# Kernel optimization log

Measured on AMD Instinct MI355X. Metric: run time of the kernel, lower is better.

## Reference

```python
import jax, jax.numpy as jnp
import numpy as np

B = 4_194_304  # batch size


def setup_inputs() -> dict:
    key = jax.random.key(0)
    k1, k2, k3, k4 = jax.random.split(key, 4)
    X = jax.random.normal(k1, (B, 4), dtype=jnp.float32)
    mu = jax.random.normal(k2, (B, 2), dtype=jnp.float32)
    sigma = jax.random.uniform(k3, (B,), dtype=jnp.float32)
    u = jax.random.normal(k4, (B, 2), dtype=jnp.float32)
    Q = jnp.array([[1.0, 0.0, 0.0, 0.0],
                   [0.0, 1.0, 0.0, 0.0],
                   [0.0, 0.0, 0.5, 0.0],
                   [0.0, 0.0, 0.0, 0.5]], dtype=jnp.float32)
    R = jnp.array([[0.1, 0.0], [0.0, 0.1]], dtype=jnp.float32)
    x_target = jnp.array([1.0, 0.0, 0.0, 0.0], dtype=jnp.float32)
    return {"X": X, "mu": mu, "sigma": sigma, "u": u,
            "Q": Q, "R": R, "x_target": x_target}


def reference(X, mu, sigma, u, Q, R, x_target):
    omega = 0.6
    # Hard-coded system matrices from HJBModel.__init__
    f = jnp.array([[0.0, 0.0, 1.0, 0.0],
                   [0.0, 0.0, 0.0, 1.0],
                   [0.0, omega, 0.0, 0.0],
                   [-omega, 0.0, 0.0, 0.0]], dtype=X.dtype)
    G = jnp.array([[0.3, 0.0], [0.0, 0.25], [1.0, 0.0], [0.0, 1.0]], dtype=X.dtype)
    COV = jnp.array([[0.0, 0.0], [0.0, 0.0], [0.5, 0.0], [0.0, 0.5]], dtype=X.dtype)

    xr = X - x_target                                    # [B,4]
    # V = xr^T Q xr
    V = jnp.einsum('bi,ij,bj->b', xr, Q, xr)             # [B]
    # dyn = f X + G u + COV mu
    dyn = X @ f.T + u @ G.T + mu @ COV.T                 # [B,4]
    # grad1 @ dyn = 2 xr^T Q dyn
    g1dyn = 2.0 * jnp.einsum('bi,ij,bj->b', xr, Q, dyn)  # [B]
    # 0.5 u^T R u
    uRu = 0.5 * jnp.einsum('bi,ij,bj->b', u, R, u)       # [B]
    # trace term: 0.5 sigma^2 * trace(2Q @ COV COV^T)
    tr_const = jnp.trace((2.0 * Q) @ (COV @ COV.T))      # scalar
    trace_term = 0.5 * sigma ** 2 * tr_const             # [B]
    return jnp.mean(g1dyn + V + uRu + trace_term)
```

## Files before the change

### kernel.cpp

```cpp
#include <hip/hip_runtime.h>

#define BLOCK 256
#define GRID  4096

__device__ __forceinline__ float row_val(
    float x0, float x1, float x2, float x3,
    float u0, float u1, float m0, float m1, float sg,
    const float* q, float r0, float r1, float r2, float r3,
    float t0, float t1, float t2, float t3, float tr_c)
{
    float xr0 = x0 - t0, xr1 = x1 - t1, xr2 = x2 - t2, xr3 = x3 - t3;
    float dyn0 = x2 + 0.3f * u0;
    float dyn1 = x3 + 0.25f * u1;
    float dyn2 = 0.6f * x1 + u0 + 0.5f * m0;
    float dyn3 = -0.6f * x0 + u1 + 0.5f * m1;
    float qx0 = xr0 * q[0] + xr1 * q[4] + xr2 * q[8]  + xr3 * q[12];
    float qx1 = xr0 * q[1] + xr1 * q[5] + xr2 * q[9]  + xr3 * q[13];
    float qx2 = xr0 * q[2] + xr1 * q[6] + xr2 * q[10] + xr3 * q[14];
    float qx3 = xr0 * q[3] + xr1 * q[7] + xr2 * q[11] + xr3 * q[15];
    float V    = qx0 * xr0 + qx1 * xr1 + qx2 * xr2 + qx3 * xr3;
    float g1   = 2.0f * (qx0 * dyn0 + qx1 * dyn1 + qx2 * dyn2 + qx3 * dyn3);
    float uRu  = 0.5f * (u0 * (r0 * u0 + r1 * u1) + u1 * (r2 * u0 + r3 * u1));
    float tt   = 0.5f * sg * sg * tr_c;
    return V + g1 + uRu + tt;
}

__global__ __launch_bounds__(BLOCK) void hjb_loss_kernel(
    const float* __restrict__ X,
    const float* __restrict__ mu,
    const float* __restrict__ sigma,
    const float* __restrict__ u,
    const float* __restrict__ Q,
    const float* __restrict__ R,
    const float* __restrict__ xt,
    float* __restrict__ partials,
    int B, float inv_B)
{
    float q[16];
#pragma unroll
    for (int i = 0; i < 16; ++i) q[i] = Q[i];
    const float r0 = R[0], r1 = R[1], r2 = R[2], r3 = R[3];
    const float t0 = xt[0], t1 = xt[1], t2 = xt[2], t3 = xt[3];
    const float tr_c = 0.5f * (q[10] + q[15]);

    const float4*  __restrict__ X4  = reinterpret_cast<const float4*>(X);
    const float2*  __restrict__ u2  = reinterpret_cast<const float2*>(u);
    const float2*  __restrict__ mu2 = reinterpret_cast<const float2*>(mu);

    float acc = 0.0f;
    const int tid = blockIdx.x * BLOCK + threadIdx.x;
    const int T   = gridDim.x * BLOCK;

    int r = tid;
    for (; r + 3 * T < B; r += 4 * T) {
        const int ra = r, rb = r + T, rc = r + 2 * T, rd = r + 3 * T;
        float4 xa = X4[ra];  float4 xb = X4[rb];
        float4 xc = X4[rc];  float4 xd = X4[rd];
        float2 ua = u2[ra];  float2 ub = u2[rb];
        float2 uc = u2[rc];  float2 ud = u2[rd];
        float2 ma = mu2[ra]; float2 mb = mu2[rb];
        float2 mc = mu2[rc]; float2 md = mu2[rd];
        float  sa = sigma[ra]; float sb = sigma[rb];
        float  sc = sigma[rc]; float sd = sigma[rd];

        acc += row_val(xa.x, xa.y, xa.z, xa.w, ua.x, ua.y, ma.x, ma.y, sa,
                       q, r0, r1, r2, r3, t0, t1, t2, t3, tr_c);
        acc += row_val(xb.x, xb.y, xb.z, xb.w, ub.x, ub.y, mb.x, mb.y, sb,
                       q, r0, r1, r2, r3, t0, t1, t2, t3, tr_c);
        acc += row_val(xc.x, xc.y, xc.z, xc.w, uc.x, uc.y, mc.x, mc.y, sc,
                       q, r0, r1, r2, r3, t0, t1, t2, t3, tr_c);
        acc += row_val(xd.x, xd.y, xd.z, xd.w, ud.x, ud.y, md.x, md.y, sd,
                       q, r0, r1, r2, r3, t0, t1, t2, t3, tr_c);
    }
    for (; r < B; r += T) {
        float4 x = X4[r];
        float2 uu = u2[r];
        float2 mm = mu2[r];
        float  sg = sigma[r];
        acc += row_val(x.x, x.y, x.z, x.w, uu.x, uu.y, mm.x, mm.y, sg,
                       q, r0, r1, r2, r3, t0, t1, t2, t3, tr_c);
    }

    acc *= inv_B;

#pragma unroll
    for (int off = 32; off > 0; off >>= 1)
        acc += __shfl_down(acc, off, 64);

    __shared__ float wave_sums[BLOCK / 64];
    const int lane = threadIdx.x & 63;
    const int wid  = threadIdx.x >> 6;
    if (lane == 0) wave_sums[wid] = acc;
    __syncthreads();

    if (wid == 0) {
        float v = (lane < BLOCK / 64) ? wave_sums[lane] : 0.0f;
        v += __shfl_down(v, 2, 64);
        v += __shfl_down(v, 1, 64);
        if (lane == 0) partials[blockIdx.x] = v;
    }
}

__global__ __launch_bounds__(BLOCK) void hjb_finish_kernel(
    const float* __restrict__ partials, float* __restrict__ out, int n)
{
    float acc = 0.0f;
    for (int i = threadIdx.x; i < n; i += BLOCK)
        acc += partials[i];
#pragma unroll
    for (int off = 32; off > 0; off >>= 1)
        acc += __shfl_down(acc, off, 64);

    __shared__ float wave_sums[BLOCK / 64];
    const int lane = threadIdx.x & 63;
    const int wid  = threadIdx.x >> 6;
    if (lane == 0) wave_sums[wid] = acc;
    __syncthreads();

    if (wid == 0) {
        float v = (lane < BLOCK / 64) ? wave_sums[lane] : 0.0f;
        v += __shfl_down(v, 2, 64);
        v += __shfl_down(v, 1, 64);
        if (lane == 0) out[0] = v;
    }
}

extern "C" void kernel_launch(void* const* d_in, const int* in_sizes, int n_in,
                              void* d_out, int out_size, void* d_ws, size_t ws_size,
                              hipStream_t stream) {
    const float* X     = (const float*)d_in[0];
    const float* mu    = (const float*)d_in[1];
    const float* sigma = (const float*)d_in[2];
    const float* u     = (const float*)d_in[3];
    const float* Q     = (const float*)d_in[4];
    const float* R     = (const float*)d_in[5];
    const float* xt    = (const float*)d_in[6];
    float* out = (float*)d_out;
    float* partials = (float*)d_ws;

    const int B = in_sizes[2];
    const float inv_B = 1.0f / (float)B;

    hjb_loss_kernel<<<GRID, BLOCK, 0, stream>>>(
        X, mu, sigma, u, Q, R, xt, partials, B, inv_B);
    hjb_finish_kernel<<<1, BLOCK, 0, stream>>>(partials, out, GRID);
}
```

Measured before the change: 177.0 us.

## Process row pairs per thread with wider vector loads and double the grid

```diff
diff --git a/kernel.cpp b/kernel.cpp
--- a/kernel.cpp
+++ b/kernel.cpp
@@ -1,7 +1,11 @@
 #include <hip/hip_runtime.h>
 
 #define BLOCK 256
-#define GRID  4096
+#define GRID  8192
+
+__device__ __forceinline__ float uniform_f(float v) {
+    return __int_as_float(__builtin_amdgcn_readfirstlane(__float_as_int(v)));
+}
 
 __device__ __forceinline__ float row_val(
     float x0, float x1, float x2, float x3,
@@ -25,7 +29,7 @@
     return V + g1 + uRu + tt;
 }
 
-__global__ __launch_bounds__(BLOCK) void hjb_loss_kernel(
+__global__ __launch_bounds__(BLOCK, 8) void hjb_loss_kernel(
     const float* __restrict__ X,
     const float* __restrict__ mu,
     const float* __restrict__ sigma,
@@ -34,50 +38,36 @@
     const float* __restrict__ R,
     const float* __restrict__ xt,
     float* __restrict__ partials,
-    int B, float inv_B)
+    int npairs, float inv_B)
 {
     float q[16];
 #pragma unroll
-    for (int i = 0; i < 16; ++i) q[i] = Q[i];
-    const float r0 = R[0], r1 = R[1], r2 = R[2], r3 = R[3];
-    const float t0 = xt[0], t1 = xt[1], t2 = xt[2], t3 = xt[3];
+    for (int i = 0; i < 16; ++i) q[i] = uniform_f(Q[i]);
+    const float r0 = uniform_f(R[0]), r1 = uniform_f(R[1]);
+    const float r2 = uniform_f(R[2]), r3 = uniform_f(R[3]);
+    const float t0 = uniform_f(xt[0]), t1 = uniform_f(xt[1]);
+    const float t2 = uniform_f(xt[2]), t3 = uniform_f(xt[3]);
     const float tr_c = 0.5f * (q[10] + q[15]);
 
-    const float4*  __restrict__ X4  = reinterpret_cast<const float4*>(X);
-    const float2*  __restrict__ u2  = reinterpret_cast<const float2*>(u);
-    const float2*  __restrict__ mu2 = reinterpret_cast<const float2*>(mu);
+    const float4* __restrict__ X4  = reinterpret_cast<const float4*>(X);
+    const float4* __restrict__ u4  = reinterpret_cast<const float4*>(u);
+    const float4* __restrict__ mu4 = reinterpret_cast<const float4*>(mu);
+    const float2* __restrict__ s2  = reinterpret_cast<const float2*>(sigma);
 
     float acc = 0.0f;
     const int tid = blockIdx.x * BLOCK + threadIdx.x;
     const int T   = gridDim.x * BLOCK;
 
-    int r = tid;
-    for (; r + 3 * T < B; r += 4 * T) {
-        const int ra = r, rb = r + T, rc = r + 2 * T, rd = r + 3 * T;
-        float4 xa = X4[ra];  float4 xb = X4[rb];
-        float4 xc = X4[rc];  float4 xd = X4[rd];
-        float2 ua = u2[ra];  float2 ub = u2[rb];
-        float2 uc = u2[rc];  float2 ud = u2[rd];
-        float2 ma = mu2[ra]; float2 mb = mu2[rb];
-        float2 mc = mu2[rc]; float2 md = mu2[rd];
-        float  sa = sigma[ra]; float sb = sigma[rb];
-        float  sc = sigma[rc]; float sd = sigma[rd];
+    for (int p = tid; p < npairs; p += T) {
+        float4 xa = X4[2 * p + 0];
+        float4 xb = X4[2 * p + 1];
+        float4 uu = u4[p];
+        float4 mm = mu4[p];
+        float2 ss = s2[p];
 
-        acc += row_val(xa.x, xa.y, xa.z, xa.w, ua.x, ua.y, ma.x, ma.y, sa,
+        acc += row_val(xa.x, xa.y, xa.z, xa.w, uu.x, uu.y, mm.x, mm.y, ss.x,
                        q, r0, r1, r2, r3, t0, t1, t2, t3, tr_c);
-        acc += row_val(xb.x, xb.y, xb.z, xb.w, ub.x, ub.y, mb.x, mb.y, sb,
-                       q, r0, r1, r2, r3, t0, t1, t2, t3, tr_c);
-        acc += row_val(xc.x, xc.y, xc.z, xc.w, uc.x, uc.y, mc.x, mc.y, sc,
-                       q, r0, r1, r2, r3, t0, t1, t2, t3, tr_c);
-        acc += row_val(xd.x, xd.y, xd.z, xd.w, ud.x, ud.y, md.x, md.y, sd,
-                       q, r0, r1, r2, r3, t0, t1, t2, t3, tr_c);
-    }
-    for (; r < B; r += T) {
-        float4 x = X4[r];
-        float2 uu = u2[r];
-        float2 mm = mu2[r];
-        float  sg = sigma[r];
-        acc += row_val(x.x, x.y, x.z, x.w, uu.x, uu.y, mm.x, mm.y, sg,
+        acc += row_val(xb.x, xb.y, xb.z, xb.w, uu.z, uu.w, mm.z, mm.w, ss.y,
                        q, r0, r1, r2, r3, t0, t1, t2, t3, tr_c);
     }
 
@@ -139,9 +129,10 @@
     float* partials = (float*)d_ws;
 
     const int B = in_sizes[2];
+    const int npairs = B / 2;
     const float inv_B = 1.0f / (float)B;
 
     hjb_loss_kernel<<<GRID, BLOCK, 0, stream>>>(
-        X, mu, sigma, u, Q, R, xt, partials, B, inv_B);
+        X, mu, sigma, u, Q, R, xt, partials, npairs, inv_B);
     hjb_finish_kernel<<<1, BLOCK, 0, stream>>>(partials, out, GRID);
 }
```

Measured after the change: 175.0 us. No clear change (-1.2%).
